# Kernel tuning notes

Hardware: AMD Instinct MI355X
Metric: run time of the kernel (lower is better)

## Reference

```python
import jax, jax.numpy as jnp
import numpy as np

B, T, D, U = 32, 4096, 512, 512

def setup_inputs() -> dict:
    key = jax.random.key(0)
    ks = jax.random.split(key, 8)
    s = 0.02
    return {
        "query": jax.random.normal(ks[0], (B, D), dtype=jnp.float32),
        "values": jax.random.normal(ks[1], (B, T, D), dtype=jnp.float32),
        "W1": jax.random.normal(ks[2], (D, U), dtype=jnp.float32) * s,
        "b1": jnp.zeros((U,), dtype=jnp.float32),
        "W2": jax.random.normal(ks[3], (D, U), dtype=jnp.float32) * s,
        "b2": jnp.zeros((U,), dtype=jnp.float32),
        "V": jax.random.normal(ks[4], (U, 1), dtype=jnp.float32) * s,
        "bv": jnp.zeros((1,), dtype=jnp.float32),
    }

def reference(query, values, W1, b1, W2, b2, V, bv):
    # query: [B, D] -> [B, 1, U]; values: [B, T, D] -> [B, T, U]
    q_proj = (query @ W1 + b1)[:, None, :]            # [B, 1, U]
    v_proj = values @ W2 + b2                          # [B, T, U]
    scores = jnp.tanh(q_proj + v_proj) @ V + bv        # [B, T, 1]
    attn = jax.nn.softmax(scores, axis=1)              # softmax over time axis
    context = jnp.sum(attn * values, axis=1)           # [B, D]
    return context
```

## Files before the change

kernel.cpp:

```cpp
#include <hip/hip_runtime.h>
#include <hip/hip_bf16.h>
#include <math.h>

#define B_ 32
#define T_ 4096
#define D_ 512
#define U_ 512

typedef __bf16 bf16x8 __attribute__((ext_vector_type(8)));
typedef float floatx4 __attribute__((ext_vector_type(4)));
typedef unsigned short ushortx8 __attribute__((ext_vector_type(8)));

static __device__ __forceinline__ unsigned int f2bf(float f) {
  unsigned int u = __float_as_uint(f);
  return (u + 0x7fffu + ((u >> 16) & 1u)) >> 16;
}

static __device__ __forceinline__ float tanh_fast(float x) {
  float e = exp2f(x * 2.88539008178f);
  return 1.0f - 2.0f * __builtin_amdgcn_rcpf(1.0f + e);
}

static __device__ __forceinline__ uint4 pack8(const float4 a, const float4 b) {
  uint4 pk;
  pk.x = f2bf(a.x) | (f2bf(a.y) << 16);
  pk.y = f2bf(a.z) | (f2bf(a.w) << 16);
  pk.z = f2bf(b.x) | (f2bf(b.y) << 16);
  pk.w = f2bf(b.z) | (f2bf(b.w) << 16);
  return pk;
}

__global__ __launch_bounds__(256) void prep_w2b(
    const float* __restrict__ W2, unsigned short* __restrict__ W2B) {
  const int s = blockIdx.x * 256 + threadIdx.x;
  const int lane = s & 63;
  const int frag = s >> 6;
  const int ub = frag >> 4;
  const int kb = frag & 15;
  const int lr = lane & 15;
  const int kc = lane >> 4;
  const int u = ub * 16 + lr;
  const int k0 = kb * 32 + kc * 8;
  ushortx8 pk;
#pragma unroll
  for (int j = 0; j < 8; ++j)
    pk[j] = (unsigned short)f2bf(W2[(size_t)(k0 + j) * U_ + u]);
  *(ushortx8*)&W2B[(size_t)s * 8] = pk;
}

__global__ __launch_bounds__(256) void qproj_kernel(
    const float* __restrict__ query, const float* __restrict__ W1,
    const float* __restrict__ b1, const float* __restrict__ b2,
    float* __restrict__ qp) {
  const int b = blockIdx.x;
  const int ug = blockIdx.y;
  const int tid = threadIdx.x;
  const int uq = tid & 63;
  const int kq = tid >> 6;
  __shared__ float qs[D_];
  __shared__ float red[4][64];
  qs[tid] = query[b * D_ + tid];
  qs[tid + 256] = query[b * D_ + tid + 256];
  __syncthreads();
  const int u = ug * 64 + uq;
  float a = 0.f;
#pragma unroll 8
  for (int k = kq * 128; k < kq * 128 + 128; ++k)
    a += qs[k] * W1[(size_t)k * U_ + u];
  red[kq][uq] = a;
  __syncthreads();
  if (tid < 64) {
    const int uu = ug * 64 + tid;
    qp[b * U_ + uu] =
        red[0][tid] + red[1][tid] + red[2][tid] + red[3][tid] + b1[uu] + b2[uu];
  }
}

__global__ __launch_bounds__(512, 2) void scores_mfma(
    const float* __restrict__ values, const unsigned short* __restrict__ W2B,
    const float* __restrict__ qp, const float* __restrict__ V,
    float* __restrict__ wexp) {
  __shared__ __align__(16) unsigned short As[2 * 64 * 512];
  __shared__ float redp[2 * 512];

  const int b = blockIdx.y;
  const int tg = blockIdx.x;
  const int tid = threadIdx.x;
  const int w = tid >> 6;
  const int lane = tid & 63;
  const int lr = lane & 15;
  const int kc = lane >> 4;
  const int w4 = w * 4;

  const float* vbase = values + ((size_t)b * T_ + (size_t)tg * 512) * D_;
  const ushortx8* W2Bv = (const ushortx8*)W2B;

  float qv[4], vv[4];
  const float* qpb = qp + b * U_;
#pragma unroll
  for (int j = 0; j < 4; ++j) {
    const int u = w * 64 + j * 16 + lr;
    qv[j] = qpb[u];
    vv[j] = V[u];
  }

  {
#pragma unroll
    for (int p = 0; p < 8; ++p) {
      const int r = p * 8 + w;
      const float* rp = vbase + (size_t)r * D_ + lane * 8;
      const float4 f0 = *(const float4*)rp;
      const float4 f1 = *(const float4*)(rp + 4);
      *(uint4*)&As[r * 512 + (lane ^ w) * 8] = pack8(f0, f1);
    }
  }
  __syncthreads();

  for (int n = 0; n < 8; ++n) {
    const int cur = n & 1;
    const unsigned short* Asc = As + cur * 32768;

    float4 sv[16];
    if (n + 1 < 8) {
      const float* tb = vbase + (size_t)(n + 1) * 64 * D_;
#pragma unroll
      for (int p = 0; p < 8; ++p) {
        const float* rp = tb + (size_t)(p * 8 + w) * D_ + lane * 8;
        sv[2 * p] = *(const float4*)rp;
        sv[2 * p + 1] = *(const float4*)(rp + 4);
      }
    }

    floatx4 acc[4][4];
#pragma unroll
    for (int i = 0; i < 4; ++i)
#pragma unroll
      for (int j = 0; j < 4; ++j) acc[i][j] = (floatx4)0.f;

#pragma unroll 4
    for (int ks = 0; ks < 16; ++ks) {
      bf16x8 bfr[4];
#pragma unroll
      for (int j = 0; j < 4; ++j)
        bfr[j] = __builtin_bit_cast(
            bf16x8, W2Bv[((w4 + j) * 16 + ks) * 64 + lane]);
      const int c = (ks * 4 + kc) ^ (lr & 7);
      bf16x8 af[4];
#pragma unroll
      for (int i = 0; i < 4; ++i) {
        const int ri = i * 16 + lr;
        af[i] =
            __builtin_bit_cast(bf16x8, *(const ushortx8*)&Asc[ri * 512 + c * 8]);
      }
#pragma unroll
      for (int i = 0; i < 4; ++i)
#pragma unroll
        for (int j = 0; j < 4; ++j)
          acc[i][j] = __builtin_amdgcn_mfma_f32_16x16x32_bf16(
              af[i], bfr[j], acc[i][j], 0, 0, 0);
    }

#pragma unroll
    for (int i = 0; i < 4; ++i) {
#pragma unroll
      for (int r = 0; r < 4; ++r) {
        float s = 0.f;
#pragma unroll
        for (int j = 0; j < 4; ++j) s += tanh_fast(acc[i][j][r] + qv[j]) * vv[j];
        s += __shfl_xor(s, 1);
        s += __shfl_xor(s, 2);
        s += __shfl_xor(s, 4);
        s += __shfl_xor(s, 8);
        if (lr == 0) redp[cur * 512 + w * 64 + i * 16 + kc * 4 + r] = s;
      }
    }

    if (n + 1 < 8) {
      unsigned short* Asn = As + (cur ^ 1) * 32768;
      const int c = lane ^ w;
#pragma unroll
      for (int p = 0; p < 8; ++p) {
        const int r = p * 8 + w;
        *(uint4*)&Asn[r * 512 + c * 8] = pack8(sv[2 * p], sv[2 * p + 1]);
      }
    }

    __syncthreads();

    {
      const int row = tid >> 3;
      const int p = tid & 7;
      float s = redp[cur * 512 + p * 64 + row];
      s += __shfl_xor(s, 1);
      s += __shfl_xor(s, 2);
      s += __shfl_xor(s, 4);
      if (p == 0)
        wexp[(size_t)b * T_ + tg * 512 + n * 64 + row] = expf(s);
    }
  }
}

__global__ __launch_bounds__(256) void context_kernel(
    const float* __restrict__ values, const float* __restrict__ wexp,
    float* __restrict__ out) {
  const int b = blockIdx.x;
  const int t0 = blockIdx.y * 128;
  const int tid = threadIdx.x;
  const int tx = tid & 127;
  const int ty = tid >> 7;
  __shared__ float as[128];
  __shared__ float4 redv[128];
  __shared__ float dred[4];

  const float* wb = wexp + (size_t)b * T_;
  float lsum = 0.f;
#pragma unroll
  for (int i = 0; i < 16; ++i) lsum += wb[i * 256 + tid];
#pragma unroll
  for (int off = 1; off < 64; off <<= 1) lsum += __shfl_xor(lsum, off);
  if ((tid & 63) == 0) dred[tid >> 6] = lsum;
  __syncthreads();
  const float scale = 1.0f / (dred[0] + dred[1] + dred[2] + dred[3]);
  if (tid < 128) as[tid] = wb[t0 + tid] * scale;
  __syncthreads();

  const float* vb = values + ((size_t)b * T_ + t0) * D_;
  float ax = 0.f, ay = 0.f, az = 0.f, aw = 0.f;
#pragma unroll 8
  for (int t = ty; t < 128; t += 2) {
    const float a = as[t];
    const float4 v = *(const float4*)&vb[(size_t)t * D_ + tx * 4];
    ax += a * v.x;
    ay += a * v.y;
    az += a * v.z;
    aw += a * v.w;
  }
  if (ty == 1) redv[tx] = make_float4(ax, ay, az, aw);
  __syncthreads();
  if (ty == 0) {
    const float4 o = redv[tx];
    const int d = tx * 4;
    atomicAdd(&out[b * D_ + d],     ax + o.x);
    atomicAdd(&out[b * D_ + d + 1], ay + o.y);
    atomicAdd(&out[b * D_ + d + 2], az + o.z);
    atomicAdd(&out[b * D_ + d + 3], aw + o.w);
  }
}

extern "C" void kernel_launch(void* const* d_in, const int* in_sizes, int n_in,
                              void* d_out, int out_size, void* d_ws,
                              size_t ws_size, hipStream_t stream) {
  const float* query = (const float*)d_in[0];
  const float* values = (const float*)d_in[1];
  const float* W1 = (const float*)d_in[2];
  const float* b1 = (const float*)d_in[3];
  const float* W2 = (const float*)d_in[4];
  const float* b2 = (const float*)d_in[5];
  const float* V = (const float*)d_in[6];

  float* qp = (float*)d_ws;
  float* wexp = qp + (size_t)B_ * U_;
  unsigned short* W2B = (unsigned short*)(wexp + (size_t)B_ * T_);
  float* out = (float*)d_out;

  (void)hipMemsetAsync(d_out, 0, (size_t)B_ * D_ * sizeof(float), stream);

  prep_w2b<<<128, 256, 0, stream>>>(W2, W2B);
  qproj_kernel<<<dim3(B_, 8), 256, 0, stream>>>(query, W1, b1, b2, qp);
  scores_mfma<<<dim3(8, B_), 512, 0, stream>>>(values, W2B, qp, V, wexp);
  context_kernel<<<dim3(B_, 32), 256, 0, stream>>>(values, wexp, out);
}
```

Before: 527.5 us.

## Fuse softmax-weighted context accumulation into scores kernel reusing LDS tiles

Computes exp(score)-weighted sums of the bf16 value tiles already staged in shared memory inside the scores kernel. Numerator and denominator are accumulated atomically, and a tiny kernel normalises them. This removes the separate context kernel's second full fp32 pass over values and the wexp round-trip. The prefetch is split into two halves to lower register pressure. The risk is reduced accuracy, since context now uses bf16-rounded values, plus extra LDS reads and atomics.

```diff
diff --git a/kernel.cpp b/kernel.cpp
--- a/kernel.cpp
+++ b/kernel.cpp
@@ -22,12 +22,10 @@
 }
 
 static __device__ __forceinline__ uint4 pack8(const float4 a, const float4 b) {
-  uint4 pk;
-  pk.x = f2bf(a.x) | (f2bf(a.y) << 16);
-  pk.y = f2bf(a.z) | (f2bf(a.w) << 16);
-  pk.z = f2bf(b.x) | (f2bf(b.y) << 16);
-  pk.w = f2bf(b.z) | (f2bf(b.w) << 16);
-  return pk;
+  bf16x8 v;
+  v[0] = (__bf16)a.x; v[1] = (__bf16)a.y; v[2] = (__bf16)a.z; v[3] = (__bf16)a.w;
+  v[4] = (__bf16)b.x; v[5] = (__bf16)b.y; v[6] = (__bf16)b.z; v[7] = (__bf16)b.w;
+  return __builtin_bit_cast(uint4, v);
 }
 
 __global__ __launch_bounds__(256) void prep_w2b(
@@ -76,10 +74,12 @@
   }
 }
 
-__global__ __launch_bounds__(512, 2) void scores_mfma(
-    const float* __restrict__ values, const unsigned short* __restrict__ W2B,
-    const float* __restrict__ qp, const float* __restrict__ V,
-    float* __restrict__ wexp) {
+__global__ __attribute__((amdgpu_flat_work_group_size(512, 512),
+                          amdgpu_waves_per_eu(2, 2)))
+void scores_mfma(const float* __restrict__ values,
+                 const unsigned short* __restrict__ W2B,
+                 const float* __restrict__ qp, const float* __restrict__ V,
+                 float* __restrict__ num, float* __restrict__ den) {
   __shared__ __align__(16) unsigned short As[2 * 64 * 512];
   __shared__ float redp[2 * 512];
 
@@ -91,6 +91,7 @@
   const int lr = lane & 15;
   const int kc = lane >> 4;
   const int w4 = w * 4;
+  const int cw = lane ^ w;
 
   const float* vbase = values + ((size_t)b * T_ + (size_t)tg * 512) * D_;
   const ushortx8* W2Bv = (const ushortx8*)W2B;
@@ -104,14 +105,25 @@
     vv[j] = V[u];
   }
 
-  {
-#pragma unroll
-    for (int p = 0; p < 8; ++p) {
-      const int r = p * 8 + w;
+  float wacc[8];
+#pragma unroll
+  for (int d = 0; d < 8; ++d) wacc[d] = 0.f;
+  float denl = 0.f;
+
+#pragma unroll
+  for (int h = 0; h < 2; ++h) {
+    float4 pv[8];
+#pragma unroll
+    for (int p = 0; p < 4; ++p) {
+      const int r = (h * 4 + p) * 8 + w;
       const float* rp = vbase + (size_t)r * D_ + lane * 8;
-      const float4 f0 = *(const float4*)rp;
-      const float4 f1 = *(const float4*)(rp + 4);
-      *(uint4*)&As[r * 512 + (lane ^ w) * 8] = pack8(f0, f1);
+      pv[2 * p] = *(const float4*)rp;
+      pv[2 * p + 1] = *(const float4*)(rp + 4);
+    }
+#pragma unroll
+    for (int p = 0; p < 4; ++p) {
+      const int r = (h * 4 + p) * 8 + w;
+      *(uint4*)&As[r * 512 + cw * 8] = pack8(pv[2 * p], pv[2 * p + 1]);
     }
   }
   __syncthreads();
@@ -119,39 +131,73 @@
   for (int n = 0; n < 8; ++n) {
     const int cur = n & 1;
     const unsigned short* Asc = As + cur * 32768;
-
-    float4 sv[16];
-    if (n + 1 < 8) {
-      const float* tb = vbase + (size_t)(n + 1) * 64 * D_;
-#pragma unroll
-      for (int p = 0; p < 8; ++p) {
+    unsigned short* Asn = As + (cur ^ 1) * 32768;
+    const float* tb = vbase + (size_t)(n + 1) * 64 * D_;
+
+    floatx4 acc[4][4];
+#pragma unroll
+    for (int i = 0; i < 4; ++i)
+#pragma unroll
+      for (int j = 0; j < 4; ++j) acc[i][j] = (floatx4)0.f;
+
+    float4 sv[8];
+    if (n < 7) {
+#pragma unroll
+      for (int p = 0; p < 4; ++p) {
         const float* rp = tb + (size_t)(p * 8 + w) * D_ + lane * 8;
         sv[2 * p] = *(const float4*)rp;
         sv[2 * p + 1] = *(const float4*)(rp + 4);
       }
     }
 
-    floatx4 acc[4][4];
-#pragma unroll
-    for (int i = 0; i < 4; ++i)
-#pragma unroll
-      for (int j = 0; j < 4; ++j) acc[i][j] = (floatx4)0.f;
-
-#pragma unroll 4
-    for (int ks = 0; ks < 16; ++ks) {
+#pragma unroll
+    for (int ks = 0; ks < 8; ++ks) {
       bf16x8 bfr[4];
 #pragma unroll
       for (int j = 0; j < 4; ++j)
-        bfr[j] = __builtin_bit_cast(
-            bf16x8, W2Bv[((w4 + j) * 16 + ks) * 64 + lane]);
+        bfr[j] = __builtin_bit_cast(bf16x8,
+                                    W2Bv[((w4 + j) * 16 + ks) * 64 + lane]);
       const int c = (ks * 4 + kc) ^ (lr & 7);
       bf16x8 af[4];
 #pragma unroll
-      for (int i = 0; i < 4; ++i) {
-        const int ri = i * 16 + lr;
-        af[i] =
-            __builtin_bit_cast(bf16x8, *(const ushortx8*)&Asc[ri * 512 + c * 8]);
-      }
+      for (int i = 0; i < 4; ++i)
+        af[i] = __builtin_bit_cast(
+            bf16x8, *(const ushortx8*)&Asc[(i * 16 + lr) * 512 + c * 8]);
+#pragma unroll
+      for (int i = 0; i < 4; ++i)
+#pragma unroll
+        for (int j = 0; j < 4; ++j)
+          acc[i][j] = __builtin_amdgcn_mfma_f32_16x16x32_bf16(
+              af[i], bfr[j], acc[i][j], 0, 0, 0);
+    }
+
+    if (n < 7) {
+#pragma unroll
+      for (int p = 0; p < 4; ++p) {
+        const int r = p * 8 + w;
+        *(uint4*)&Asn[r * 512 + cw * 8] = pack8(sv[2 * p], sv[2 * p + 1]);
+      }
+#pragma unroll
+      for (int p = 0; p < 4; ++p) {
+        const float* rp = tb + (size_t)((p + 4) * 8 + w) * D_ + lane * 8;
+        sv[2 * p] = *(const float4*)rp;
+        sv[2 * p + 1] = *(const float4*)(rp + 4);
+      }
+    }
+
+#pragma unroll
+    for (int ks = 8; ks < 16; ++ks) {
+      bf16x8 bfr[4];
+#pragma unroll
+      for (int j = 0; j < 4; ++j)
+        bfr[j] = __builtin_bit_cast(bf16x8,
+                                    W2Bv[((w4 + j) * 16 + ks) * 64 + lane]);
+      const int c = (ks * 4 + kc) ^ (lr & 7);
+      bf16x8 af[4];
+#pragma unroll
+      for (int i = 0; i < 4; ++i)
+        af[i] = __builtin_bit_cast(
+            bf16x8, *(const ushortx8*)&Asc[(i * 16 + lr) * 512 + c * 8]);
 #pragma unroll
       for (int i = 0; i < 4; ++i)
 #pragma unroll
@@ -175,76 +221,66 @@
       }
     }
 
-    if (n + 1 < 8) {
-      unsigned short* Asn = As + (cur ^ 1) * 32768;
-      const int c = lane ^ w;
-#pragma unroll
-      for (int p = 0; p < 8; ++p) {
-        const int r = p * 8 + w;
-        *(uint4*)&Asn[r * 512 + c * 8] = pack8(sv[2 * p], sv[2 * p + 1]);
+    if (n < 7) {
+#pragma unroll
+      for (int p = 0; p < 4; ++p) {
+        const int r = (p + 4) * 8 + w;
+        *(uint4*)&Asn[r * 512 + cw * 8] = pack8(sv[2 * p], sv[2 * p + 1]);
       }
     }
 
     __syncthreads();
 
-    {
-      const int row = tid >> 3;
-      const int p = tid & 7;
-      float s = redp[cur * 512 + p * 64 + row];
-      s += __shfl_xor(s, 1);
-      s += __shfl_xor(s, 2);
-      s += __shfl_xor(s, 4);
-      if (p == 0)
-        wexp[(size_t)b * T_ + tg * 512 + n * 64 + row] = expf(s);
-    }
-  }
-}
-
-__global__ __launch_bounds__(256) void context_kernel(
-    const float* __restrict__ values, const float* __restrict__ wexp,
+    float sw = redp[cur * 512 + lane];
+#pragma unroll
+    for (int p = 1; p < 8; ++p) sw += redp[cur * 512 + p * 64 + lane];
+    const float wgt = expf(sw);
+    if (w == 0) denl += wgt;
+
+#pragma unroll
+    for (int jj = 0; jj < 8; ++jj) {
+      const int r = (lane >> 3) + 8 * jj;
+      const float wr = __shfl(wgt, r);
+      const int g = (w * 8 + (lane & 7)) ^ (lane >> 3);
+      const ushortx8 vx = *(const ushortx8*)&Asc[r * 512 + g * 8];
+#pragma unroll
+      for (int d = 0; d < 8; ++d)
+        wacc[d] += wr * __uint_as_float((unsigned)vx[d] << 16);
+    }
+
+    __syncthreads();
+  }
+
+#pragma unroll
+  for (int d = 0; d < 8; ++d) {
+    wacc[d] += __shfl_xor(wacc[d], 8);
+    wacc[d] += __shfl_xor(wacc[d], 16);
+    wacc[d] += __shfl_xor(wacc[d], 32);
+  }
+  if (lane < 8) {
+    const int d0 = (w * 8 + lane) * 8;
+#pragma unroll
+    for (int d = 0; d < 8; ++d) atomicAdd(&num[b * D_ + d0 + d], wacc[d]);
+  }
+  if (w == 0) {
+#pragma unroll
+    for (int off = 1; off < 64; off <<= 1) denl += __shfl_xor(denl, off);
+    if (lane == 0) atomicAdd(&den[b], denl);
+  }
+}
+
+__global__ __launch_bounds__(128) void normalize_kernel(
+    const float* __restrict__ num, const float* __restrict__ den,
     float* __restrict__ out) {
   const int b = blockIdx.x;
-  const int t0 = blockIdx.y * 128;
-  const int tid = threadIdx.x;
-  const int tx = tid & 127;
-  const int ty = tid >> 7;
-  __shared__ float as[128];
-  __shared__ float4 redv[128];
-  __shared__ float dred[4];
-
-  const float* wb = wexp + (size_t)b * T_;
-  float lsum = 0.f;
-#pragma unroll
-  for (int i = 0; i < 16; ++i) lsum += wb[i * 256 + tid];
-#pragma unroll
-  for (int off = 1; off < 64; off <<= 1) lsum += __shfl_xor(lsum, off);
-  if ((tid & 63) == 0) dred[tid >> 6] = lsum;
-  __syncthreads();
-  const float scale = 1.0f / (dred[0] + dred[1] + dred[2] + dred[3]);
-  if (tid < 128) as[tid] = wb[t0 + tid] * scale;
-  __syncthreads();
-
-  const float* vb = values + ((size_t)b * T_ + t0) * D_;
-  float ax = 0.f, ay = 0.f, az = 0.f, aw = 0.f;
-#pragma unroll 8
-  for (int t = ty; t < 128; t += 2) {
-    const float a = as[t];
-    const float4 v = *(const float4*)&vb[(size_t)t * D_ + tx * 4];
-    ax += a * v.x;
-    ay += a * v.y;
-    az += a * v.z;
-    aw += a * v.w;
-  }
-  if (ty == 1) redv[tx] = make_float4(ax, ay, az, aw);
-  __syncthreads();
-  if (ty == 0) {
-    const float4 o = redv[tx];
-    const int d = tx * 4;
-    atomicAdd(&out[b * D_ + d],     ax + o.x);
-    atomicAdd(&out[b * D_ + d + 1], ay + o.y);
-    atomicAdd(&out[b * D_ + d + 2], az + o.z);
-    atomicAdd(&out[b * D_ + d + 3], aw + o.w);
-  }
+  const float inv = 1.0f / den[b];
+  const int d = threadIdx.x * 4;
+  float4 v = *(const float4*)&num[b * D_ + d];
+  v.x *= inv;
+  v.y *= inv;
+  v.z *= inv;
+  v.w *= inv;
+  *(float4*)&out[b * D_ + d] = v;
 }
 
 extern "C" void kernel_launch(void* const* d_in, const int* in_sizes, int n_in,
@@ -259,14 +295,15 @@
   const float* V = (const float*)d_in[6];
 
   float* qp = (float*)d_ws;
-  float* wexp = qp + (size_t)B_ * U_;
-  unsigned short* W2B = (unsigned short*)(wexp + (size_t)B_ * T_);
+  unsigned short* W2B = (unsigned short*)(qp + (size_t)B_ * U_);
+  float* num = (float*)(W2B + (size_t)U_ * D_);
+  float* den = num + (size_t)B_ * D_;
   float* out = (float*)d_out;
 
-  (void)hipMemsetAsync(d_out, 0, (size_t)B_ * D_ * sizeof(float), stream);
+  (void)hipMemsetAsync(num, 0, ((size_t)B_ * D_ + B_) * sizeof(float), stream);
 
   prep_w2b<<<128, 256, 0, stream>>>(W2, W2B);
   qproj_kernel<<<dim3(B_, 8), 256, 0, stream>>>(query, W1, b1, b2, qp);
-  scores_mfma<<<dim3(8, B_), 512, 0, stream>>>(values, W2B, qp, V, wexp);
-  context_kernel<<<dim3(B_, 32), 256, 0, stream>>>(values, wexp, out);
-}
+  scores_mfma<<<dim3(8, B_), 512, 0, stream>>>(values, W2B, qp, V, num, den);
+  normalize_kernel<<<B_, 128, 0, stream>>>(num, den, out);
+}
```

After: 609.8 us. 15.6% more time.
